# Performance work log

Measured on AMD Instinct MI355X. Metric: run time of the kernel, lower is better.

## Reference

```python
import jax, jax.numpy as jnp
import numpy as np

N = 100000   # nodes
E = 1600000  # edges
R = 500      # relation types
D = 128      # in_ent_feats == out_ent_feats
H = 8        # heads
Dh = 16      # head dim
DFF = 4 * D  # feed-forward hidden
HOPS = 5
ALPHA = 0.15
SLOPE = 0.2
EPS = 1e-5


def setup_inputs() -> dict:
    key = jax.random.key(0)
    ks = jax.random.split(key, 12)
    s = 0.05  # small-init scale
    return {
        "ent_feat": jax.random.normal(ks[0], (N, D), jnp.float32),
        "rel_feat": jax.random.normal(ks[1], (R, D), jnp.float32),
        "src": jax.random.randint(ks[2], (E,), 0, N),
        "dst": jax.random.randint(ks[3], (E,), 0, N),
        "e_type": jax.random.randint(ks[4], (E,), 0, R),
        "ln1_g": jnp.ones((D,), jnp.float32),
        "ln1_b": jnp.zeros((D,), jnp.float32),
        "W_ent": jax.random.normal(ks[5], (D, H * Dh), jnp.float32) * s,
        "W_rel": jax.random.normal(ks[6], (D, H * Dh), jnp.float32) * s,
        "attn_h": jax.random.normal(ks[7], (1, H, Dh), jnp.float32) * s,
        "attn_t": jax.random.normal(ks[8], (1, H, Dh), jnp.float32) * s,
        "attn_r": jax.random.normal(ks[9], (1, H, Dh), jnp.float32) * s,
        "ln2_g": jnp.ones((H * Dh,), jnp.float32),
        "ln2_b": jnp.zeros((H * Dh,), jnp.float32),
        "W1": jax.random.normal(ks[10], (H * Dh, DFF), jnp.float32) * s,
        "b1": jnp.zeros((DFF,), jnp.float32),
        "W2": jax.random.normal(ks[11], (DFF, H * Dh), jnp.float32) * s,
        "b2": jnp.zeros((H * Dh,), jnp.float32),
    }


def _ln(x, g, b):
    mu = x.mean(-1, keepdims=True)
    var = x.var(-1, keepdims=True)
    return (x - mu) * jax.lax.rsqrt(var + EPS) * g + b


def reference(ent_feat, rel_feat, src, dst, e_type,
              ln1_g, ln1_b, W_ent, W_rel, attn_h, attn_t, attn_r,
              ln2_g, ln2_b, W1, b1, W2, b2):
    # graph layer norm (dropout is identity at eval)
    h = _ln(ent_feat, ln1_g, ln1_b)                       # [N, D]
    feat = (h @ W_ent).reshape(N, H, Dh)                  # [N, H, Dh]
    frel = (rel_feat @ W_rel).reshape(R, H, Dh)           # [R, H, Dh]
    eh = (feat * attn_h).sum(-1)                          # [N, H]
    et = (feat * attn_t).sum(-1)                          # [N, H]
    er = (frel * attn_r).sum(-1)[e_type]                  # [E, H]
    # edge scores: u_add_v + relation term, leaky relu
    e = eh[src] + et[dst] + er                            # [E, H]
    e = jnp.where(e > 0, e, SLOPE * e)
    # edge softmax over incoming edges of each dst node
    m = jax.ops.segment_max(e, dst, num_segments=N)       # [N, H]
    ex = jnp.exp(e - m[dst])
    ssum = jax.ops.segment_sum(ex, dst, num_segments=N)
    a = ex / ssum[dst]                                    # [E, H]
    # PPR diffusion
    feat0 = feat
    f = feat0
    for _ in range(HOPS):
        msg = f[src] * a[:, :, None]                      # [E, H, Dh]
        agg = jax.ops.segment_sum(msg, dst, num_segments=N)
        f = (1.0 - ALPHA) * agg + ALPHA * feat0
    # residual (Identity since in == out)
    rst = f + h.reshape(N, H, Dh)
    rst = rst.reshape(N, H * Dh)
    # feed-forward sublayer with residual
    y = _ln(rst, ln2_g, ln2_b)
    ff = jax.nn.relu(y @ W1 + b1) @ W2 + b2
    return ff + rst
```

## Files before the change

kernel.cpp:

```cpp
#include <hip/hip_runtime.h>
#include <hip/hip_bf16.h>
#include <math.h>

#define N_NODES 100000
#define N_EDGES 1600000
#define N_REL   500
#define DIM     128
#define NHEAD   8
#define DFF     512
#define ALPHA   0.15f
#define SLOPE   0.2f
#define LN_EPS  1e-5f

#define SCHUNK   1024
#define NSCANBLK ((N_NODES + SCHUNK - 1) / SCHUNK)

#define NWIN    8
#define WNODES  12500
#define NECHUNK 256
#define ECHUNK  (N_EDGES / NECHUNK)

typedef unsigned short u16;
typedef unsigned int   u32;

typedef __attribute__((ext_vector_type(8))) short  bf16x8;
typedef __attribute__((ext_vector_type(4))) float  f32x4;

__device__ __forceinline__ float bf2f(u16 u) {
    return __uint_as_float(((u32)u) << 16);
}
__device__ __forceinline__ u16 f2bf(float f) {
    __hip_bfloat16 b = __float2bfloat16(f);
    return *reinterpret_cast<u16*>(&b);
}

__device__ __forceinline__ void fma_row(float* acc, float a, const bf16x8& r) {
    const u32* w = (const u32*)&r;
#pragma unroll
    for (int jj = 0; jj < 4; ++jj) {
        acc[2 * jj]     += a * __uint_as_float(w[jj] << 16);
        acc[2 * jj + 1] += a * __uint_as_float(w[jj] & 0xffff0000u);
    }
}

__global__ void zero_k(int* __restrict__ p, int n) {
    int i = blockIdx.x * blockDim.x + threadIdx.x;
    if (i < n) p[i] = 0;
}

__global__ void swz1_k(const float* __restrict__ W1, u16* __restrict__ W1s) {
    const int i = blockIdx.x * 256 + threadIdx.x;
    const int k = i >> 9, n = i & 511;
    W1s[n * DIM + k] = f2bf(W1[i]);
}
__global__ void swz2_k(const float* __restrict__ W2, u16* __restrict__ W2s) {
    const int i = blockIdx.x * 256 + threadIdx.x;
    const int k = i >> 7, n = i & 127;
    W2s[n * DFF + k] = f2bf(W2[i]);
}
__global__ void swze_k(const float* __restrict__ W, u16* __restrict__ Ws) {
    const int i = blockIdx.x * 256 + threadIdx.x;
    const int k = i >> 7, n = i & 127;
    Ws[n * DIM + k] = f2bf(W[i]);
}

__global__ __launch_bounds__(128) void ln1_k(const float* __restrict__ x,
        const float* __restrict__ g, const float* __restrict__ b,
        u16* __restrict__ h) {
    const int n = blockIdx.x, t = threadIdx.x;
    const float v = x[n * DIM + t];
    float s = v, q = v * v;
#pragma unroll
    for (int off = 32; off > 0; off >>= 1) {
        s += __shfl_xor(s, off, 64);
        q += __shfl_xor(q, off, 64);
    }
    __shared__ float ss[2], qq[2];
    if ((t & 63) == 0) { ss[t >> 6] = s; qq[t >> 6] = q; }
    __syncthreads();
    s = ss[0] + ss[1]; q = qq[0] + qq[1];
    const float mu  = s * (1.0f / 128.0f);
    const float var = q * (1.0f / 128.0f) - mu * mu;
    const float rs  = rsqrtf(fmaxf(var, 0.f) + LN_EPS);
    h[n * DIM + t] = f2bf((v - mu) * rs * g[t] + b[t]);
}

#define HP 136
__global__ __launch_bounds__(256) void proj_k(const u16* __restrict__ h,
        const u16* __restrict__ Wes,
        u16* __restrict__ feat0) {
    __shared__ u16 hsb[32 * HP];
    const int t   = threadIdx.x;
    const int n0b = blockIdx.x * 32;

    {
        const int sr = t >> 3;
        const int sc = (t & 7) * 16;
        const u16* hrow = &h[(size_t)(n0b + sr) * DIM + sc];
        u16* drow = &hsb[sr * HP + sc];
        ((uint4*)drow)[0] = ((const uint4*)hrow)[0];
        ((uint4*)drow)[1] = ((const uint4*)hrow)[1];
    }
    __syncthreads();

    const int wv   = t >> 6;
    const int lane = t & 63;
    const int lm   = lane & 15;
    const int q4   = lane >> 4;
    const int mrow = (wv & 1) * 16;
    const int chalf = (wv >> 1) * 64;

    bf16x8 afr[4];
#pragma unroll
    for (int kt = 0; kt < 4; ++kt)
        afr[kt] = *(const bf16x8*)&hsb[(mrow + lm) * HP + kt * 32 + q4 * 8];

#pragma unroll
    for (int nt = 0; nt < 4; ++nt) {
        const int c0 = chalf + nt * 16;
        f32x4 acc = {0.f, 0.f, 0.f, 0.f};
#pragma unroll
        for (int kt = 0; kt < 4; ++kt) {
            const bf16x8 bfr = *(const bf16x8*)&Wes[(c0 + lm) * DIM + kt * 32 + q4 * 8];
            acc = __builtin_amdgcn_mfma_f32_16x16x32_bf16(afr[kt], bfr, acc, 0, 0, 0);
        }
#pragma unroll
        for (int r = 0; r < 4; ++r)
            feat0[(size_t)(n0b + mrow + q4 * 4 + r) * DIM + c0 + lm] = f2bf(acc[r]);
    }
}

__global__ __launch_bounds__(256) void eh_k(const u16* __restrict__ feat0,
        const float* __restrict__ attn_h, const float* __restrict__ attn_t,
        float* __restrict__ eh, float* __restrict__ et) {
    __shared__ float ahs[DIM], ats[DIM];
    const int t = threadIdx.x;
    if (t < DIM) { ahs[t] = attn_h[t]; ats[t] = attn_t[t]; }
    __syncthreads();
    const int idx  = blockIdx.x * 256 + t;
    const int n    = idx >> 3;
    const int head = idx & 7;
    const u16* fp = &feat0[(size_t)n * DIM + head * 16];
    float sh = 0.f, st = 0.f;
#pragma unroll
    for (int i = 0; i < 4; ++i) {
        const ushort4 f4 = ((const ushort4*)fp)[i];
        const int c = head * 16 + i * 4;
        sh += bf2f(f4.x) * ahs[c+0] + bf2f(f4.y) * ahs[c+1]
            + bf2f(f4.z) * ahs[c+2] + bf2f(f4.w) * ahs[c+3];
        st += bf2f(f4.x) * ats[c+0] + bf2f(f4.y) * ats[c+1]
            + bf2f(f4.z) * ats[c+2] + bf2f(f4.w) * ats[c+3];
    }
    eh[idx] = sh;
    et[idx] = st;
}

__global__ __launch_bounds__(128) void rel_k(const float* __restrict__ rel_feat,
        const float* __restrict__ W,
        const float* __restrict__ attn_r, float* __restrict__ er) {
    __shared__ float rf[DIM];
    __shared__ float pr[DIM];
    const int r = blockIdx.x, t = threadIdx.x;
    rf[t] = rel_feat[r * DIM + t];
    __syncthreads();
    float acc = 0.f;
    for (int d = 0; d < DIM; ++d) acc += rf[d] * W[d * DIM + t];
    pr[t] = acc * attn_r[t];
    __syncthreads();
    if (t < NHEAD) {
        float s = 0.f;
        for (int i = 0; i < 16; ++i) s += pr[t * 16 + i];
        er[r * NHEAD + t] = s;
    }
}

__global__ void count_k(const int* __restrict__ dst, int* __restrict__ counts) {
    int e = blockIdx.x * blockDim.x + threadIdx.x;
    if (e < N_EDGES) atomicAdd(&counts[dst[e]], 1);
}

__global__ __launch_bounds__(256) void scan1_k(const int* __restrict__ counts,
        int* __restrict__ offsets, int* __restrict__ blk_sums, int n) {
    __shared__ int wsum[4];
    const int t = threadIdx.x, lane = t & 63, wid = t >> 6;
    const int base = blockIdx.x * SCHUNK + t * 4;
    int v0 = 0, v1 = 0, v2 = 0, v3 = 0;
    if (base + 3 < n) {
        const int4 c4 = *(const int4*)&counts[base];
        v0 = c4.x; v1 = c4.y; v2 = c4.z; v3 = c4.w;
    } else {
        if (base + 0 < n) v0 = counts[base + 0];
        if (base + 1 < n) v1 = counts[base + 1];
        if (base + 2 < n) v2 = counts[base + 2];
        if (base + 3 < n) v3 = counts[base + 3];
    }
    const int s4 = v0 + v1 + v2 + v3;
    int incl = s4;
#pragma unroll
    for (int off = 1; off < 64; off <<= 1) {
        const int tt = __shfl_up(incl, off, 64);
        if (lane >= off) incl += tt;
    }
    if (lane == 63) wsum[wid] = incl;
    __syncthreads();
    int wbase = 0;
#pragma unroll
    for (int w = 0; w < 4; ++w) if (w < wid) wbase += wsum[w];
    const int excl = wbase + incl - s4;
    if (base + 0 < n) offsets[base + 0] = excl;
    if (base + 1 < n) offsets[base + 1] = excl + v0;
    if (base + 2 < n) offsets[base + 2] = excl + v0 + v1;
    if (base + 3 < n) offsets[base + 3] = excl + v0 + v1 + v2;
    if (t == 255) blk_sums[blockIdx.x] = wbase + incl;
}

__global__ __launch_bounds__(128) void scan2_k(const int* __restrict__ blk_sums,
        int* __restrict__ blk_off, int* __restrict__ offsets, int nblk, int n) {
    const int t = threadIdx.x;
    const int v = (t < nblk) ? blk_sums[t] : 0;
    int incl = v;
#pragma unroll
    for (int off = 1; off < 64; off <<= 1) {
        const int tt = __shfl_up(incl, off, 64);
        if ((t & 63) >= off) incl += tt;
    }
    __shared__ int w0sum;
    if (t == 63) w0sum = incl;
    __syncthreads();
    int x = incl - v;
    if (t >= 64) x += w0sum;
    if (t < nblk) blk_off[t] = x;
    if (t == nblk - 1) offsets[n] = x + v;
}

__global__ __launch_bounds__(256) void scan3_k(int* __restrict__ offsets,
        int* __restrict__ cursor, const int* __restrict__ blk_off, int n) {
    const int add  = blk_off[blockIdx.x];
    const int base = blockIdx.x * SCHUNK + threadIdx.x * 4;
#pragma unroll
    for (int j = 0; j < 4; ++j) {
        const int i = base + j;
        if (i < n) {
            const int o = offsets[i] + add;
            offsets[i] = o;
            cursor[i]  = o;
        }
    }
}

__global__ __launch_bounds__(256) void scatter_k(const int* __restrict__ src,
        const int* __restrict__ dst, const int* __restrict__ etype,
        int* __restrict__ cursor, u32* __restrict__ csr_se) {
    const int b  = blockIdx.x;
    const int w  = b & (NWIN - 1);
    const int r  = b >> 3;
    const int lo = w * WNODES, hi = lo + WNODES;
    const int base = r * ECHUNK;
    for (int i = threadIdx.x; i < ECHUNK; i += 256) {
        const int e = base + i;
        const int d = dst[e];
        if (d >= lo && d < hi) {
            const int s   = src[e];
            const int rel = etype[e];
            const int pos = atomicAdd(&cursor[d], 1);
            if (pos >= 0 && pos < N_EDGES)
                csr_se[pos] = (u32)s | ((u32)rel << 17);
        }
    }
}

__global__ __launch_bounds__(256) void softmax_k(const int* __restrict__ offsets,
        const u32* __restrict__ csr_se,
        const float* __restrict__ eh, const float* __restrict__ et,
        const float* __restrict__ er,
        u16* __restrict__ csr_ab, float* __restrict__ inv_buf) {
    const int n = blockIdx.x * 4 + (threadIdx.x >> 6);
    const int beg = offsets[n], end = offsets[n + 1];
    const int lane = threadIdx.x & 63;
    const int k  = lane & 7;
    const int eo = lane >> 3;
    const float etk = et[n * NHEAD + k];
    float m = -1e30f;
    for (int e = beg + eo; e < end; e += 8) {
        const u32 se = csr_se[e];
        const int s = se & 0x1FFFF;
        const int r = se >> 17;
        float sc = eh[s * NHEAD + k] + etk + er[r * NHEAD + k];
        sc = sc > 0.f ? sc : SLOPE * sc;
        m = fmaxf(m, sc);
    }
    m = fmaxf(m, __shfl_xor(m, 8, 64));
    m = fmaxf(m, __shfl_xor(m, 16, 64));
    m = fmaxf(m, __shfl_xor(m, 32, 64));
    float ssum = 0.f;
    for (int e = beg + eo; e < end; e += 8) {
        const u32 se = csr_se[e];
        const int s = se & 0x1FFFF;
        const int r = se >> 17;
        float sc = eh[s * NHEAD + k] + etk + er[r * NHEAD + k];
        sc = sc > 0.f ? sc : SLOPE * sc;
        const float ex = expf(sc - m);
        csr_ab[(size_t)e * NHEAD + k] = f2bf(ex);
        ssum += ex;
    }
    ssum += __shfl_xor(ssum, 8, 64);
    ssum += __shfl_xor(ssum, 16, 64);
    ssum += __shfl_xor(ssum, 32, 64);
    const float inv = 1.f / fmaxf(ssum, 1e-20f);
    if (lane < 8) inv_buf[n * NHEAD + lane] = inv;
}

__global__ __launch_bounds__(256) void hop_k(const u16* __restrict__ f_in,
        u16* __restrict__ f_out, const u16* __restrict__ feat0,
        const int* __restrict__ offsets, const u32* __restrict__ csr_se,
        const u16* __restrict__ csr_ab, const float* __restrict__ inv_buf) {
    const int n    = blockIdx.x * 4 + (threadIdx.x >> 6);
    const int lane = threadIdx.x & 63;
    const int li   = lane & 15;
    const int grp  = lane >> 4;
    const int hsel = li >> 1;
    const int beg = offsets[n], end = offsets[n + 1];

    float acc[8];
#pragma unroll
    for (int j = 0; j < 8; ++j) acc[j] = 0.f;

#define LOADM(E, IDX, S_, A_)                                            \
    {                                                                    \
        const int eu = (E) + 4 * (IDX) + grp;                            \
        S_ = csr_se[eu] & 0x1FFFF;                                       \
        const float av = bf2f(csr_ab[(size_t)eu * NHEAD + hsel]);        \
        A_ = (eu < end) ? av : 0.f;                                      \
    }

    int e0 = beg;
    u32 s0 = 0, s1 = 0, s2 = 0, s3 = 0;
    float a0 = 0.f, a1 = 0.f, a2 = 0.f, a3 = 0.f;
    if (e0 < end) {
        LOADM(e0, 0, s0, a0); LOADM(e0, 1, s1, a1);
        LOADM(e0, 2, s2, a2); LOADM(e0, 3, s3, a3);
    }
    for (; e0 < end; e0 += 16) {
        u32 t0 = 0, t1 = 0, t2 = 0, t3 = 0;
        float b0 = 0.f, b1 = 0.f, b2 = 0.f, b3 = 0.f;
        if (e0 + 16 < end) {
            LOADM(e0 + 16, 0, t0, b0); LOADM(e0 + 16, 1, t1, b1);
            LOADM(e0 + 16, 2, t2, b2); LOADM(e0 + 16, 3, t3, b3);
        }
        const bf16x8 r0 = *(const bf16x8*)&f_in[(size_t)s0 * DIM + li * 8];
        const bf16x8 r1 = *(const bf16x8*)&f_in[(size_t)s1 * DIM + li * 8];
        const bf16x8 r2 = *(const bf16x8*)&f_in[(size_t)s2 * DIM + li * 8];
        const bf16x8 r3 = *(const bf16x8*)&f_in[(size_t)s3 * DIM + li * 8];
        fma_row(acc, a0, r0);
        fma_row(acc, a1, r1);
        fma_row(acc, a2, r2);
        fma_row(acc, a3, r3);
        s0 = t0; s1 = t1; s2 = t2; s3 = t3;
        a0 = b0; a1 = b1; a2 = b2; a3 = b3;
    }
#undef LOADM
#pragma unroll
    for (int j = 0; j < 8; ++j) {
        acc[j] += __shfl_xor(acc[j], 16, 64);
        acc[j] += __shfl_xor(acc[j], 32, 64);
    }
    if (lane < 16) {
        const float iv = inv_buf[n * NHEAD + hsel];
        const bf16x8 p = *(const bf16x8*)&feat0[(size_t)n * DIM + li * 8];
        bf16x8 o;
#pragma unroll
        for (int j = 0; j < 8; ++j)
            o[j] = (short)f2bf((1.f - ALPHA) * acc[j] * iv + ALPHA * bf2f((u16)p[j]));
        *(bf16x8*)&f_out[(size_t)n * DIM + li * 8] = o;
    }
}

#define YP 136
#define ZP 520
__global__ __launch_bounds__(256) void ffn_k(const u16* __restrict__ f,
        const u16* __restrict__ h,
        const float* __restrict__ g2, const float* __restrict__ b2ln,
        const u16* __restrict__ W1s,
        const float* __restrict__ b1,
        const u16* __restrict__ W2s,
        const float* __restrict__ b2,
        float* __restrict__ out) {
    __shared__ u16 ysb[32 * YP];
    __shared__ u16 zsb[32 * ZP];

    const int t    = threadIdx.x;
    const int n0b  = blockIdx.x * 32;
    const int wv   = t >> 6;
    const int lane = t & 63;

    {
        const int nl   = lane >> 3;
        const int node = wv * 8 + nl;
        const int cp   = (lane & 7) * 16;
        const int gbase = (n0b + node) * DIM + cp;
        float rv[16];
#pragma unroll
        for (int i = 0; i < 4; ++i) {
            const ushort4 fu = *(const ushort4*)&f[gbase + i * 4];
            const ushort4 hu = *(const ushort4*)&h[gbase + i * 4];
            rv[i * 4 + 0] = bf2f(fu.x) + bf2f(hu.x);
            rv[i * 4 + 1] = bf2f(fu.y) + bf2f(hu.y);
            rv[i * 4 + 2] = bf2f(fu.z) + bf2f(hu.z);
            rv[i * 4 + 3] = bf2f(fu.w) + bf2f(hu.w);
        }
        float s = 0.f, q = 0.f;
#pragma unroll
        for (int i = 0; i < 16; ++i) { s += rv[i]; q += rv[i] * rv[i]; }
        s += __shfl_xor(s, 1, 64); q += __shfl_xor(q, 1, 64);
        s += __shfl_xor(s, 2, 64); q += __shfl_xor(q, 2, 64);
        s += __shfl_xor(s, 4, 64); q += __shfl_xor(q, 4, 64);
        const float mu  = s * (1.0f / 128.0f);
        const float var = q * (1.0f / 128.0f) - mu * mu;
        const float rs  = rsqrtf(fmaxf(var, 0.f) + LN_EPS);
#pragma unroll
        for (int i = 0; i < 4; ++i) {
            ushort4 yo;
            const int c = cp + i * 4;
            yo.x = f2bf((rv[i*4+0] - mu) * rs * g2[c+0] + b2ln[c+0]);
            yo.y = f2bf((rv[i*4+1] - mu) * rs * g2[c+1] + b2ln[c+1]);
            yo.z = f2bf((rv[i*4+2] - mu) * rs * g2[c+2] + b2ln[c+2]);
            yo.w = f2bf((rv[i*4+3] - mu) * rs * g2[c+3] + b2ln[c+3]);
            *(ushort4*)&ysb[node * YP + c] = yo;
        }
    }
    __syncthreads();

    const int lm = lane & 15;
    const int q4 = lane >> 4;

    {
        bf16x8 afr[2][4];
#pragma unroll
        for (int mt = 0; mt < 2; ++mt)
#pragma unroll
            for (int kt = 0; kt < 4; ++kt)
                afr[mt][kt] = *(const bf16x8*)&ysb[(mt * 16 + lm) * YP + kt * 32 + q4 * 8];

        const int cw = wv * 128;
        bf16x8 bc[4];
#pragma unroll
        for (int kt = 0; kt < 4; ++kt)
            bc[kt] = *(const bf16x8*)&W1s[(cw + lm) * DIM + kt * 32 + q4 * 8];

#pragma unroll
        for (int nt = 0; nt < 8; ++nt) {
            const int n0 = cw + nt * 16;
            bf16x8 bn[4] = {bc[0], bc[1], bc[2], bc[3]};
            if (nt < 7) {
#pragma unroll
                for (int kt = 0; kt < 4; ++kt)
                    bn[kt] = *(const bf16x8*)&W1s[(n0 + 16 + lm) * DIM + kt * 32 + q4 * 8];
            }
            f32x4 acc0 = {0.f, 0.f, 0.f, 0.f};
            f32x4 acc1 = {0.f, 0.f, 0.f, 0.f};
#pragma unroll
            for (int kt = 0; kt < 4; ++kt) {
                acc0 = __builtin_amdgcn_mfma_f32_16x16x32_bf16(afr[0][kt], bc[kt], acc0, 0, 0, 0);
                acc1 = __builtin_amdgcn_mfma_f32_16x16x32_bf16(afr[1][kt], bc[kt], acc1, 0, 0, 0);
            }
            const float bias = b1[n0 + lm];
#pragma unroll
            for (int r = 0; r < 4; ++r) {
                zsb[(q4 * 4 + r) * ZP + n0 + lm]      = f2bf(fmaxf(acc0[r] + bias, 0.f));
                zsb[(16 + q4 * 4 + r) * ZP + n0 + lm] = f2bf(fmaxf(acc1[r] + bias, 0.f));
            }
#pragma unroll
            for (int kt = 0; kt < 4; ++kt) bc[kt] = bn[kt];
        }
    }
    __syncthreads();

    f32x4 acc[2][2];
#pragma unroll
    for (int i = 0; i < 2; ++i)
#pragma unroll
        for (int j = 0; j < 2; ++j)
            acc[i][j] = (f32x4){0.f, 0.f, 0.f, 0.f};
    const int c0 = wv * 32;
    bf16x8 wc0 = *(const bf16x8*)&W2s[(c0 + lm) * DFF + q4 * 8];
    bf16x8 wc1 = *(const bf16x8*)&W2s[(c0 + 16 + lm) * DFF + q4 * 8];
#pragma unroll
    for (int kt = 0; kt < 16; ++kt) {
        bf16x8 wn0 = wc0, wn1 = wc1;
        if (kt < 15) {
            wn0 = *(const bf16x8*)&W2s[(c0 + lm) * DFF + (kt + 1) * 32 + q4 * 8];
            wn1 = *(const bf16x8*)&W2s[(c0 + 16 + lm) * DFF + (kt + 1) * 32 + q4 * 8];
        }
        const bf16x8 a0 = *(const bf16x8*)&zsb[(lm) * ZP + kt * 32 + q4 * 8];
        const bf16x8 a1 = *(const bf16x8*)&zsb[(16 + lm) * ZP + kt * 32 + q4 * 8];
        acc[0][0] = __builtin_amdgcn_mfma_f32_16x16x32_bf16(a0, wc0, acc[0][0], 0, 0, 0);
        acc[0][1] = __builtin_amdgcn_mfma_f32_16x16x32_bf16(a0, wc1, acc[0][1], 0, 0, 0);
        acc[1][0] = __builtin_amdgcn_mfma_f32_16x16x32_bf16(a1, wc0, acc[1][0], 0, 0, 0);
        acc[1][1] = __builtin_amdgcn_mfma_f32_16x16x32_bf16(a1, wc1, acc[1][1], 0, 0, 0);
        wc0 = wn0; wc1 = wn1;
    }

#pragma unroll
    for (int ntile = 0; ntile < 2; ++ntile) {
        const int col = c0 + ntile * 16 + lm;
        const float bias = b2[col];
#pragma unroll
        for (int mt = 0; mt < 2; ++mt) {
#pragma unroll
            for (int r = 0; r < 4; ++r) {
                const int row  = mt * 16 + q4 * 4 + r;
                const int gidx = (n0b + row) * DIM + col;
                out[gidx] = acc[mt][ntile][r] + bias + bf2f(f[gidx]) + bf2f(h[gidx]);
            }
        }
    }
}

extern "C" void kernel_launch(void* const* d_in, const int* in_sizes, int n_in,
                              void* d_out, int out_size, void* d_ws, size_t ws_size,
                              hipStream_t stream) {
    const float* ent_feat = (const float*)d_in[0];
    const float* rel_feat = (const float*)d_in[1];
    const int*   src      = (const int*)d_in[2];
    const int*   dst      = (const int*)d_in[3];
    const int*   e_type   = (const int*)d_in[4];
    const float* ln1_g    = (const float*)d_in[5];
    const float* ln1_b    = (const float*)d_in[6];
    const float* W_ent    = (const float*)d_in[7];
    const float* W_rel    = (const float*)d_in[8];
    const float* attn_h   = (const float*)d_in[9];
    const float* attn_t   = (const float*)d_in[10];
    const float* attn_r   = (const float*)d_in[11];
    const float* ln2_g    = (const float*)d_in[12];
    const float* ln2_b    = (const float*)d_in[13];
    const float* W1       = (const float*)d_in[14];
    const float* b1       = (const float*)d_in[15];
    const float* W2       = (const float*)d_in[16];
    const float* b2       = (const float*)d_in[17];
    float* out = (float*)d_out;

    char* ws = (char*)d_ws;
    size_t used = 0;
    auto alloc = [&](size_t bytes) -> char* {
        char* p = ws + used;
        used += (bytes + 255) & ~(size_t)255;
        return p;
    };
    u16*   h       = (u16*)  alloc((size_t)N_NODES * DIM * 2);
    u16*   feat0   = (u16*)  alloc((size_t)N_NODES * DIM * 2);
    u16*   fA      = (u16*)  alloc((size_t)N_NODES * DIM * 2);
    u16*   fB      = (u16*)  alloc((size_t)N_NODES * DIM * 2);
    u16*   csr_ab  = (u16*)  alloc((size_t)N_EDGES * NHEAD * 2);
    float* eh      = (float*)alloc((size_t)N_NODES * NHEAD * 4);
    float* et      = (float*)alloc((size_t)N_NODES * NHEAD * 4);
    float* inv_buf = (float*)alloc((size_t)N_NODES * NHEAD * 4);
    u32*   csr_se  = (u32*)  alloc((size_t)N_EDGES * 4);
    int*   counts  = (int*)  alloc((size_t)N_NODES * 4);
    int*   offsets = (int*)  alloc((size_t)(N_NODES + 1) * 4);
    int*   cursor  = (int*)  alloc((size_t)N_NODES * 4);
    float* er      = (float*)alloc((size_t)N_REL * NHEAD * 4);
    u16*   W1s     = (u16*)  alloc((size_t)DIM * DFF * 2);
    u16*   W2s     = (u16*)  alloc((size_t)DFF * DIM * 2);
    u16*   Wes     = (u16*)  alloc((size_t)DIM * DIM * 2);
    int*   blk_sums= (int*)  alloc((size_t)NSCANBLK * 4);
    int*   blk_off = (int*)  alloc((size_t)NSCANBLK * 4);

    if (used > ws_size) return;

    swz1_k<<<DIM * DFF / 256, 256, 0, stream>>>(W1, W1s);
    swz2_k<<<DFF * DIM / 256, 256, 0, stream>>>(W2, W2s);
    swze_k<<<DIM * DIM / 256, 256, 0, stream>>>(W_ent, Wes);

    ln1_k<<<N_NODES, 128, 0, stream>>>(ent_feat, ln1_g, ln1_b, h);
    proj_k<<<N_NODES / 32, 256, 0, stream>>>(h, Wes, feat0);
    eh_k<<<N_NODES * NHEAD / 256, 256, 0, stream>>>(feat0, attn_h, attn_t, eh, et);
    rel_k<<<N_REL, 128, 0, stream>>>(rel_feat, W_rel, attn_r, er);

    zero_k<<<(N_NODES + 255) / 256, 256, 0, stream>>>(counts, N_NODES);
    count_k<<<(N_EDGES + 255) / 256, 256, 0, stream>>>(dst, counts);
    scan1_k<<<NSCANBLK, 256, 0, stream>>>(counts, offsets, blk_sums, N_NODES);
    scan2_k<<<1, 128, 0, stream>>>(blk_sums, blk_off, offsets, NSCANBLK, N_NODES);
    scan3_k<<<NSCANBLK, 256, 0, stream>>>(offsets, cursor, blk_off, N_NODES);
    scatter_k<<<NECHUNK * NWIN, 256, 0, stream>>>(src, dst, e_type,
                                                  cursor, csr_se);
    softmax_k<<<N_NODES / 4, 256, 0, stream>>>(offsets, csr_se, eh, et, er,
                                               csr_ab, inv_buf);

    hop_k<<<N_NODES / 4, 256, 0, stream>>>(feat0, fA, feat0, offsets, csr_se, csr_ab, inv_buf);
    hop_k<<<N_NODES / 4, 256, 0, stream>>>(fA, fB, feat0, offsets, csr_se, csr_ab, inv_buf);
    hop_k<<<N_NODES / 4, 256, 0, stream>>>(fB, fA, feat0, offsets, csr_se, csr_ab, inv_buf);
    hop_k<<<N_NODES / 4, 256, 0, stream>>>(fA, fB, feat0, offsets, csr_se, csr_ab, inv_buf);
    hop_k<<<N_NODES / 4, 256, 0, stream>>>(fB, fA, feat0, offsets, csr_se, csr_ab, inv_buf);

    ffn_k<<<N_NODES / 32, 256, 0, stream>>>(fA, h, ln2_g, ln2_b, W1s, b1, W2s, b2,
                                            out);
}
```

Measured before the change: 880.0 us.

## Store node features and attention weights head-major and split hops per head

Node features and edge attention weights are stored in a head-major layout, so each head's features form a contiguous [N,16] slab. The hop kernel now gives each block a single head and a group of 16 nodes, gathering 32-byte slices per edge from a much smaller per-head working set. The goal is to make the random neighbour gathers more cache-friendly. The trade-off is reading the CSR index array once per head, issuing smaller gathers, and losing the explicit prefetch pipelining.

New measurement: 1.031 ms. 1.17x slower.

```diff
diff --git a/kernel.cpp b/kernel.cpp
--- a/kernel.cpp
+++ b/kernel.cpp
@@ -20,6 +20,8 @@
 #define NECHUNK 256
 #define ECHUNK  (N_EDGES / NECHUNK)
 
+#define N16 ((size_t)N_NODES * 16)
+
 typedef unsigned short u16;
 typedef unsigned int   u32;
 
@@ -124,9 +126,10 @@
             const bf16x8 bfr = *(const bf16x8*)&Wes[(c0 + lm) * DIM + kt * 32 + q4 * 8];
             acc = __builtin_amdgcn_mfma_f32_16x16x32_bf16(afr[kt], bfr, acc, 0, 0, 0);
         }
+        const size_t sl = (size_t)(c0 >> 4) * N16;
 #pragma unroll
         for (int r = 0; r < 4; ++r)
-            feat0[(size_t)(n0b + mrow + q4 * 4 + r) * DIM + c0 + lm] = f2bf(acc[r]);
+            feat0[sl + (size_t)(n0b + mrow + q4 * 4 + r) * 16 + lm] = f2bf(acc[r]);
     }
 }
 
@@ -140,7 +143,7 @@
     const int idx  = blockIdx.x * 256 + t;
     const int n    = idx >> 3;
     const int head = idx & 7;
-    const u16* fp = &feat0[(size_t)n * DIM + head * 16];
+    const u16* fp = &feat0[(size_t)head * N16 + (size_t)n * 16];
     float sh = 0.f, st = 0.f;
 #pragma unroll
     for (int i = 0; i < 4; ++i) {
@@ -273,13 +276,14 @@
         const u32* __restrict__ csr_se,
         const float* __restrict__ eh, const float* __restrict__ et,
         const float* __restrict__ er,
-        u16* __restrict__ csr_ab, float* __restrict__ inv_buf) {
+        u16* __restrict__ ab_hm, float* __restrict__ inv_buf) {
     const int n = blockIdx.x * 4 + (threadIdx.x >> 6);
     const int beg = offsets[n], end = offsets[n + 1];
     const int lane = threadIdx.x & 63;
     const int k  = lane & 7;
     const int eo = lane >> 3;
     const float etk = et[n * NHEAD + k];
+    u16* abk = &ab_hm[(size_t)k * N_EDGES];
     float m = -1e30f;
     for (int e = beg + eo; e < end; e += 8) {
         const u32 se = csr_se[e];
@@ -300,7 +304,7 @@
         float sc = eh[s * NHEAD + k] + etk + er[r * NHEAD + k];
         sc = sc > 0.f ? sc : SLOPE * sc;
         const float ex = expf(sc - m);
-        csr_ab[(size_t)e * NHEAD + k] = f2bf(ex);
+        abk[e] = f2bf(ex);
         ssum += ex;
     }
     ssum += __shfl_xor(ssum, 8, 64);
@@ -313,65 +317,48 @@
 __global__ __launch_bounds__(256) void hop_k(const u16* __restrict__ f_in,
         u16* __restrict__ f_out, const u16* __restrict__ feat0,
         const int* __restrict__ offsets, const u32* __restrict__ csr_se,
-        const u16* __restrict__ csr_ab, const float* __restrict__ inv_buf) {
-    const int n    = blockIdx.x * 4 + (threadIdx.x >> 6);
-    const int lane = threadIdx.x & 63;
-    const int li   = lane & 15;
-    const int grp  = lane >> 4;
-    const int hsel = li >> 1;
+        const u16* __restrict__ ab_hm, const float* __restrict__ inv_buf) {
+    const int s    = blockIdx.x & 7;
+    const int g    = blockIdx.x >> 3;
+    const int t    = threadIdx.x;
+    const int wv   = t >> 6;
+    const int lane = t & 63;
+    const int q    = lane >> 4;
+    const int eidx = (lane & 15) >> 1;
+    const int half = lane & 1;
+    const int n    = g * 16 + wv * 4 + q;
     const int beg = offsets[n], end = offsets[n + 1];
+    const u16* fsl = &f_in[(size_t)s * N16];
+    const u16* ab  = &ab_hm[(size_t)s * N_EDGES];
 
     float acc[8];
 #pragma unroll
     for (int j = 0; j < 8; ++j) acc[j] = 0.f;
 
-#define LOADM(E, IDX, S_, A_)                                            \
-    {                                                                    \
-        const int eu = (E) + 4 * (IDX) + grp;                            \
-        S_ = csr_se[eu] & 0x1FFFF;                                       \
-        const float av = bf2f(csr_ab[(size_t)eu * NHEAD + hsel]);        \
-        A_ = (eu < end) ? av : 0.f;                                      \
-    }
-
-    int e0 = beg;
-    u32 s0 = 0, s1 = 0, s2 = 0, s3 = 0;
-    float a0 = 0.f, a1 = 0.f, a2 = 0.f, a3 = 0.f;
-    if (e0 < end) {
-        LOADM(e0, 0, s0, a0); LOADM(e0, 1, s1, a1);
-        LOADM(e0, 2, s2, a2); LOADM(e0, 3, s3, a3);
-    }
-    for (; e0 < end; e0 += 16) {
-        u32 t0 = 0, t1 = 0, t2 = 0, t3 = 0;
-        float b0 = 0.f, b1 = 0.f, b2 = 0.f, b3 = 0.f;
-        if (e0 + 16 < end) {
-            LOADM(e0 + 16, 0, t0, b0); LOADM(e0 + 16, 1, t1, b1);
-            LOADM(e0 + 16, 2, t2, b2); LOADM(e0 + 16, 3, t3, b3);
-        }
-        const bf16x8 r0 = *(const bf16x8*)&f_in[(size_t)s0 * DIM + li * 8];
-        const bf16x8 r1 = *(const bf16x8*)&f_in[(size_t)s1 * DIM + li * 8];
-        const bf16x8 r2 = *(const bf16x8*)&f_in[(size_t)s2 * DIM + li * 8];
-        const bf16x8 r3 = *(const bf16x8*)&f_in[(size_t)s3 * DIM + li * 8];
-        fma_row(acc, a0, r0);
-        fma_row(acc, a1, r1);
-        fma_row(acc, a2, r2);
-        fma_row(acc, a3, r3);
-        s0 = t0; s1 = t1; s2 = t2; s3 = t3;
-        a0 = b0; a1 = b1; a2 = b2; a3 = b3;
-    }
-#undef LOADM
+    for (int e = beg + eidx; __any(e < end); e += 8) {
+        const bool vld = (e < end);
+        const int ec = vld ? e : 0;
+        const u32 se = csr_se[ec];
+        const int srcn = (int)(se & 0x1FFFF);
+        float a = bf2f(ab[ec]);
+        a = vld ? a : 0.f;
+        const bf16x8 row = *(const bf16x8*)&fsl[(size_t)srcn * 16 + half * 8];
+        fma_row(acc, a, row);
+    }
 #pragma unroll
     for (int j = 0; j < 8; ++j) {
-        acc[j] += __shfl_xor(acc[j], 16, 64);
-        acc[j] += __shfl_xor(acc[j], 32, 64);
-    }
-    if (lane < 16) {
-        const float iv = inv_buf[n * NHEAD + hsel];
-        const bf16x8 p = *(const bf16x8*)&feat0[(size_t)n * DIM + li * 8];
+        acc[j] += __shfl_xor(acc[j], 2, 64);
+        acc[j] += __shfl_xor(acc[j], 4, 64);
+        acc[j] += __shfl_xor(acc[j], 8, 64);
+    }
+    if ((lane & 15) < 2) {
+        const float iv = inv_buf[n * NHEAD + s];
+        const bf16x8 p = *(const bf16x8*)&feat0[(size_t)s * N16 + (size_t)n * 16 + half * 8];
         bf16x8 o;
 #pragma unroll
         for (int j = 0; j < 8; ++j)
             o[j] = (short)f2bf((1.f - ALPHA) * acc[j] * iv + ALPHA * bf2f((u16)p[j]));
-        *(bf16x8*)&f_out[(size_t)n * DIM + li * 8] = o;
+        *(bf16x8*)&f_out[(size_t)s * N16 + (size_t)n * 16 + half * 8] = o;
     }
 }
 
@@ -398,10 +385,11 @@
         const int node = wv * 8 + nl;
         const int cp   = (lane & 7) * 16;
         const int gbase = (n0b + node) * DIM + cp;
+        const u16* fptr = &f[(size_t)(lane & 7) * N16 + (size_t)(n0b + node) * 16];
         float rv[16];
 #pragma unroll
         for (int i = 0; i < 4; ++i) {
-            const ushort4 fu = *(const ushort4*)&f[gbase + i * 4];
+            const ushort4 fu = *(const ushort4*)&fptr[i * 4];
             const ushort4 hu = *(const ushort4*)&h[gbase + i * 4];
             rv[i * 4 + 0] = bf2f(fu.x) + bf2f(hu.x);
             rv[i * 4 + 1] = bf2f(fu.y) + bf2f(hu.y);
@@ -504,13 +492,15 @@
     for (int ntile = 0; ntile < 2; ++ntile) {
         const int col = c0 + ntile * 16 + lm;
         const float bias = b2[col];
+        const size_t fsl = (size_t)(col >> 4) * N16;
 #pragma unroll
         for (int mt = 0; mt < 2; ++mt) {
 #pragma unroll
             for (int r = 0; r < 4; ++r) {
                 const int row  = mt * 16 + q4 * 4 + r;
                 const int gidx = (n0b + row) * DIM + col;
-                out[gidx] = acc[mt][ntile][r] + bias + bf2f(f[gidx]) + bf2f(h[gidx]);
+                const float fres = bf2f(f[fsl + (size_t)(n0b + row) * 16 + (col & 15)]);
+                out[gidx] = acc[mt][ntile][r] + bias + fres + bf2f(h[gidx]);
             }
         }
     }
@@ -550,7 +540,7 @@
     u16*   feat0   = (u16*)  alloc((size_t)N_NODES * DIM * 2);
     u16*   fA      = (u16*)  alloc((size_t)N_NODES * DIM * 2);
     u16*   fB      = (u16*)  alloc((size_t)N_NODES * DIM * 2);
-    u16*   csr_ab  = (u16*)  alloc((size_t)N_EDGES * NHEAD * 2);
+    u16*   ab_hm   = (u16*)  alloc((size_t)N_EDGES * NHEAD * 2);
     float* eh      = (float*)alloc((size_t)N_NODES * NHEAD * 4);
     float* et      = (float*)alloc((size_t)N_NODES * NHEAD * 4);
     float* inv_buf = (float*)alloc((size_t)N_NODES * NHEAD * 4);
@@ -584,13 +574,14 @@
     scatter_k<<<NECHUNK * NWIN, 256, 0, stream>>>(src, dst, e_type,
                                                   cursor, csr_se);
     softmax_k<<<N_NODES / 4, 256, 0, stream>>>(offsets, csr_se, eh, et, er,
-                                               csr_ab, inv_buf);
-
-    hop_k<<<N_NODES / 4, 256, 0, stream>>>(feat0, fA, feat0, offsets, csr_se, csr_ab, inv_buf);
-    hop_k<<<N_NODES / 4, 256, 0, stream>>>(fA, fB, feat0, offsets, csr_se, csr_ab, inv_buf);
-    hop_k<<<N_NODES / 4, 256, 0, stream>>>(fB, fA, feat0, offsets, csr_se, csr_ab, inv_buf);
-    hop_k<<<N_NODES / 4, 256, 0, stream>>>(fA, fB, feat0, offsets, csr_se, csr_ab, inv_buf);
-    hop_k<<<N_NODES / 4, 256, 0, stream>>>(fB, fA, feat0, offsets, csr_se, csr_ab, inv_buf);
+                                               ab_hm, inv_buf);
+
+    const int HOPG = (N_NODES / 16) * 8;
+    hop_k<<<HOPG, 256, 0, stream>>>(feat0, fA, feat0, offsets, csr_se, ab_hm, inv_buf);
+    hop_k<<<HOPG, 256, 0, stream>>>(fA, fB, feat0, offsets, csr_se, ab_hm, inv_buf);
+    hop_k<<<HOPG, 256, 0, stream>>>(fB, fA, feat0, offsets, csr_se, ab_hm, inv_buf);
+    hop_k<<<HOPG, 256, 0, stream>>>(fA, fB, feat0, offsets, csr_se, ab_hm, inv_buf);
+    hop_k<<<HOPG, 256, 0, stream>>>(fB, fA, feat0, offsets, csr_se, ab_hm, inv_buf);
 
     ffn_k<<<N_NODES / 32, 256, 0, stream>>>(fA, h, ln2_g, ln2_b, W1s, b1, W2s, b2,
                                             out);
```
